# Kernel optimization log

Measured on AMD Instinct MI355X. Metric: run time of the kernel, lower is better.

Reference implementation:

```python
import jax, jax.numpy as jnp
import numpy as np

TAU = 0.1

def setup_inputs() -> dict:
    key = jax.random.key(0)
    kZ, k1, k2 = jax.random.split(key, 3)
    N, D = 8192, 128
    scale = 1.0 / np.sqrt(D)
    return {
        "Z": jax.random.normal(kZ, (N, D), dtype=jnp.float32),
        "W1": jax.random.normal(k1, (D, D), dtype=jnp.float32) * scale,
        "b1": jnp.zeros((D,), dtype=jnp.float32),
        "W2": jax.random.normal(k2, (D, D), dtype=jnp.float32) * scale,
        "b2": jnp.zeros((D,), dtype=jnp.float32),
    }

def reference(Z, W1, b1, W2, b2):
    # DiffusivityTransform: 2-layer MLP with ReLU (torch Linear: x @ W.T + b;
    # here W1/W2 are stored already transposed as [in, out])
    t = jax.nn.relu(Z @ W1 + b1) @ W2 + b2          # [N, D]
    sim = t @ t.T                                     # [N, N]
    S = jax.nn.softmax(sim, axis=1)                   # row-stochastic [N, N]
    Z_prop = S @ Z                                    # [N, D]
    return Z + TAU * (Z_prop - Z)
```

## Files before the change

kernel.cpp:

```cpp
#include <hip/hip_runtime.h>

typedef _Float16 half_t;
typedef _Float16 hx8 __attribute__((ext_vector_type(8)));
typedef _Float16 hx4 __attribute__((ext_vector_type(4)));
typedef float fx4 __attribute__((ext_vector_type(4)));

#define LOG2E 1.44269504088896f
#define TAU 0.1f
#define NSPLIT 8

__global__ __launch_bounds__(256) void mlpz_kernel(
    const float* __restrict__ Z, const float* __restrict__ W1,
    const float* __restrict__ b1, const float* __restrict__ W2,
    const float* __restrict__ b2, half_t* __restrict__ T,
    half_t* __restrict__ Zth)
{
  __shared__ float Ztile[64*132];
  __shared__ half_t Hs[4][16*136];
  const int tid = threadIdx.x;
  const int w = tid >> 6, lane = tid & 63;
  const int q = lane >> 4, c = lane & 15;
  const int rb = blockIdx.x*64;
  const int wrow = rb + w*16;

#pragma unroll
  for (int i=0;i<8;++i) {
    int fid = i*256 + tid;
    int r = fid >> 5, c4 = (fid & 31)*4;
    *(fx4*)(&Ztile[r*132 + c4]) = *(const fx4*)(Z + (size_t)(rb + r)*128 + c4);
  }
  __syncthreads();

  {
    const int d = tid >> 1, n0 = (tid & 1)*32;
#pragma unroll
    for (int i=0;i<4;++i) {
      hx8 hv;
#pragma unroll
      for (int u=0;u<8;++u) hv[u] = (half_t)Ztile[(n0 + i*8 + u)*132 + d];
      *(hx8*)(Zth + (size_t)d*8192 + rb + n0 + i*8) = hv;
    }
  }

  hx8 zb[4];
#pragma unroll
  for (int ks=0;ks<4;++ks) {
    fx4 a = *(const fx4*)(&Ztile[(w*16 + c)*132 + ks*32 + q*8]);
    fx4 b = *(const fx4*)(&Ztile[(w*16 + c)*132 + ks*32 + q*8 + 4]);
#pragma unroll
    for (int u=0;u<4;++u) { zb[ks][u] = (half_t)a[u]; zb[ks][4+u] = (half_t)b[u]; }
  }

  fx4 acc[8];
#pragma unroll
  for (int mt=0;mt<8;++mt) acc[mt] = (fx4){0.f,0.f,0.f,0.f};
#pragma unroll
  for (int mt=0;mt<8;++mt)
#pragma unroll
    for (int ks=0;ks<4;++ks) {
      hx8 aw;
#pragma unroll
      for (int j=0;j<8;++j)
        aw[j] = (half_t)W1[(size_t)(ks*32 + q*8 + j)*128 + mt*16 + c];
      acc[mt] = __builtin_amdgcn_mfma_f32_16x16x32_f16(aw, zb[ks], acc[mt], 0,0,0);
    }
#pragma unroll
  for (int mt=0;mt<8;++mt) {
    fx4 bias = *(const fx4*)(b1 + mt*16 + 4*q);
    hx4 hv;
#pragma unroll
    for (int i=0;i<4;++i) {
      float h = acc[mt][i] + bias[i];
      hv[i] = (half_t)(h > 0.f ? h : 0.f);
    }
    *(hx4*)(&Hs[w][c*136 + mt*16 + 4*q]) = hv;
  }

  hx8 hb[4];
#pragma unroll
  for (int ks=0;ks<4;++ks) hb[ks] = *(const hx8*)(&Hs[w][c*136 + ks*32 + q*8]);
#pragma unroll
  for (int mt=0;mt<8;++mt) acc[mt] = (fx4){0.f,0.f,0.f,0.f};
#pragma unroll
  for (int mt=0;mt<8;++mt)
#pragma unroll
    for (int ks=0;ks<4;++ks) {
      hx8 aw;
#pragma unroll
      for (int j=0;j<8;++j)
        aw[j] = (half_t)W2[(size_t)(ks*32 + q*8 + j)*128 + mt*16 + c];
      acc[mt] = __builtin_amdgcn_mfma_f32_16x16x32_f16(aw, hb[ks], acc[mt], 0,0,0);
    }
#pragma unroll
  for (int mt=0;mt<8;++mt) {
    fx4 bias = *(const fx4*)(b2 + mt*16 + 4*q);
    hx4 tv;
#pragma unroll
    for (int i=0;i<4;++i) tv[i] = (half_t)(acc[mt][i] + bias[i]);
    *(hx4*)(T + (size_t)(wrow + c)*128 + mt*16 + 4*q) = tv;
  }
}

__global__ __launch_bounds__(256,2) void flash_kernel(
    const half_t* __restrict__ T, const half_t* __restrict__ Zt,
    half_t* __restrict__ Pacc, float* __restrict__ Pm, float* __restrict__ Pl)
{
  __shared__ half_t Tbuf[2][16*512];
  __shared__ half_t Zbuf[2][16*512];
  const int tid = threadIdx.x;
  const int w = tid >> 6, lane = tid & 63;
  const int q = lane >> 4, c = lane & 15;
  const int bx = blockIdx.x;
  const int qb = bx >> 3, kh = bx & 7;
  const int wrow = qb*128 + w*32;
  const int sw = (c & 7) * 8;

  hx8 bq[2][4];
#pragma unroll
  for (int nt=0;nt<2;++nt)
#pragma unroll
    for (int ks=0;ks<4;++ks)
      bq[nt][ks] = *(const hx8*)(T + (size_t)(wrow + nt*16 + c)*128 + ks*32 + q*8);

  fx4 oacc[8][2];
#pragma unroll
  for (int mtd=0;mtd<8;++mtd)
#pragma unroll
    for (int nt=0;nt<2;++nt) oacc[mtd][nt] = (fx4){0.f,0.f,0.f,0.f};
  float m_run[2] = {-1e30f,-1e30f};
  float l_run[2] = {0.f,0.f};

  const int kbase = kh*1024;

  auto issue_loads = [&](int kt0, int b) {
    if (w < 2) {
#pragma unroll
      for (int i=0;i<8;++i) {
        int f = w*8 + i, mt = f >> 2, ks = f & 3;
        const half_t* gp = T + (size_t)(kt0 + mt*16 + c)*128 + ks*32 + q*8;
        half_t* lp = &Tbuf[b][f*512 + lane*8];
        __builtin_amdgcn_global_load_lds(
            (const __attribute__((address_space(1))) void*)gp,
            (__attribute__((address_space(3))) void*)lp, 16, 0, 0);
      }
    } else {
#pragma unroll
      for (int i=0;i<8;++i) {
        int f2 = (w-2)*8 + i, mtd = f2 >> 1, ks2 = f2 & 1;
        const half_t* gp = Zt + (size_t)(mtd*16 + c)*8192 + kt0 + ks2*32 + q*8;
        half_t* lp = &Zbuf[b][f2*512 + lane*8];
        __builtin_amdgcn_global_load_lds(
            (const __attribute__((address_space(1))) void*)gp,
            (__attribute__((address_space(3))) void*)lp, 16, 0, 0);
      }
    }
  };

  issue_loads(kbase, 0);

  for (int t=0;t<16;++t) {
    const int cur = t & 1;
    __syncthreads();
    half_t* Tcur = Tbuf[cur];
    half_t* Zcur = Zbuf[cur];
    half_t* Psw  = &Tbuf[cur][w*2048];

    fx4 sacc[4][2];
#pragma unroll
    for (int mt=0;mt<4;++mt)
#pragma unroll
      for (int nt=0;nt<2;++nt) sacc[mt][nt] = (fx4){0.f,0.f,0.f,0.f};
#pragma unroll
    for (int ks=0;ks<4;++ks)
#pragma unroll
      for (int mt=0;mt<4;++mt) {
        hx8 ak = *(const hx8*)(&Tcur[(mt*4+ks)*512 + lane*8]);
        sacc[mt][0] = __builtin_amdgcn_mfma_f32_16x16x32_f16(ak, bq[0][ks], sacc[mt][0], 0,0,0);
        sacc[mt][1] = __builtin_amdgcn_mfma_f32_16x16x32_f16(ak, bq[1][ks], sacc[mt][1], 0,0,0);
      }

    hx4 pk[2][4];
#pragma unroll
    for (int nt=0;nt<2;++nt) {
      float mx = -1e30f;
#pragma unroll
      for (int mt=0;mt<4;++mt)
#pragma unroll
        for (int i=0;i<4;++i) mx = fmaxf(mx, sacc[mt][nt][i]);
      mx = fmaxf(mx, __shfl_xor(mx, 16, 64));
      mx = fmaxf(mx, __shfl_xor(mx, 32, 64));
      float mnew = fmaxf(m_run[nt], mx);
      float alpha = __builtin_amdgcn_exp2f((m_run[nt]-mnew)*LOG2E);
      m_run[nt] = mnew;
      float nb = mnew*LOG2E;
      float rs = 0.f;
#pragma unroll
      for (int mt=0;mt<4;++mt) {
#pragma unroll
        for (int i=0;i<4;++i) {
          float p = __builtin_amdgcn_exp2f(sacc[mt][nt][i]*LOG2E - nb);
          rs += p;
          pk[nt][mt][i] = (half_t)p;
        }
      }
      rs += __shfl_xor(rs, 16, 64);
      rs += __shfl_xor(rs, 32, 64);
      l_run[nt] = l_run[nt]*alpha + rs;
#pragma unroll
      for (int mtd=0;mtd<8;++mtd)
#pragma unroll
        for (int i=0;i<4;++i) oacc[mtd][nt][i] *= alpha;
    }

    __syncthreads();
    if (t < 15) issue_loads(kbase + (t+1)*64, cur ^ 1);

#pragma unroll
    for (int nt=0;nt<2;++nt)
#pragma unroll
      for (int mt=0;mt<4;++mt)
        *(hx4*)(&Psw[(nt*16 + c)*64 + ((mt*16 + 4*q) ^ sw)]) = pk[nt][mt];

#pragma unroll
    for (int ks2=0;ks2<2;++ks2) {
      hx8 bp0 = *(const hx8*)(&Psw[(c     )*64 + ((ks2*32 + q*8) ^ sw)]);
      hx8 bp1 = *(const hx8*)(&Psw[(16 + c)*64 + ((ks2*32 + q*8) ^ sw)]);
#pragma unroll
      for (int mtd=0;mtd<8;++mtd) {
        hx8 az = *(const hx8*)(&Zcur[(mtd*2+ks2)*512 + lane*8]);
        oacc[mtd][0] = __builtin_amdgcn_mfma_f32_16x16x32_f16(az, bp0, oacc[mtd][0], 0,0,0);
        oacc[mtd][1] = __builtin_amdgcn_mfma_f32_16x16x32_f16(az, bp1, oacc[mtd][1], 0,0,0);
      }
    }
  }

#pragma unroll
  for (int nt=0;nt<2;++nt) {
    float inv = 1.0f / l_run[nt];
    const size_t rowg = (size_t)(bx*128 + w*32 + nt*16 + c);
#pragma unroll
    for (int mtd=0;mtd<8;++mtd) {
      hx4 ov;
#pragma unroll
      for (int i=0;i<4;++i) ov[i] = (half_t)(oacc[mtd][nt][i]*inv);
      *(hx4*)(Pacc + rowg*128 + mtd*16 + 4*q) = ov;
    }
    if (q == 0) {
      Pm[rowg] = m_run[nt];
      Pl[rowg] = l_run[nt];
    }
  }
}

__global__ __launch_bounds__(256) void merge_kernel(
    const float* __restrict__ Z, const half_t* __restrict__ Pacc,
    const float* __restrict__ Pm, const float* __restrict__ Pl,
    float* __restrict__ out)
{
  const int th = blockIdx.x*256 + threadIdx.x;
  const int r = th >> 5, cg = th & 31;
  const int qb = r >> 7, rr = r & 127;
  float mk[NSPLIT], lk[NSPLIT];
  float M = -1e30f;
#pragma unroll
  for (int k=0;k<NSPLIT;++k) {
    int p = qb*NSPLIT + k;
    mk[k] = Pm[p*128 + rr];
    lk[k] = Pl[p*128 + rr];
    M = fmaxf(M, mk[k]);
  }
  float L = 0.f, wk[NSPLIT];
#pragma unroll
  for (int k=0;k<NSPLIT;++k) { wk[k] = lk[k]*__builtin_amdgcn_exp2f((mk[k]-M)*LOG2E); L += wk[k]; }
  float o0=0.f,o1=0.f,o2=0.f,o3=0.f;
#pragma unroll
  for (int k=0;k<NSPLIT;++k) {
    int p = qb*NSPLIT + k;
    hx4 v = *(const hx4*)(Pacc + ((size_t)p*128 + rr)*128 + cg*4);
    o0 += wk[k]*(float)v[0]; o1 += wk[k]*(float)v[1];
    o2 += wk[k]*(float)v[2]; o3 += wk[k]*(float)v[3];
  }
  float invL = 1.0f / L;
  fx4 zv = *(const fx4*)(Z + (size_t)r*128 + cg*4);
  fx4 res;
  res[0] = (1.f-TAU)*zv[0] + TAU*o0*invL;
  res[1] = (1.f-TAU)*zv[1] + TAU*o1*invL;
  res[2] = (1.f-TAU)*zv[2] + TAU*o2*invL;
  res[3] = (1.f-TAU)*zv[3] + TAU*o3*invL;
  *(fx4*)(out + (size_t)r*128 + cg*4) = res;
}

extern "C" void kernel_launch(void* const* d_in, const int* in_sizes, int n_in,
                              void* d_out, int out_size, void* d_ws, size_t ws_size,
                              hipStream_t stream) {
  const float* Z  = (const float*)d_in[0];
  const float* W1 = (const float*)d_in[1];
  const float* b1 = (const float*)d_in[2];
  const float* W2 = (const float*)d_in[3];
  const float* b2 = (const float*)d_in[4];
  float* out = (float*)d_out;

  char* ws = (char*)d_ws;
  const size_t NBLK = 64 * NSPLIT;
  half_t* Thi  = (half_t*)(ws);
  half_t* Zth  = (half_t*)(ws + (size_t)2*1024*1024);
  half_t* Pacc = (half_t*)(ws + (size_t)4*1024*1024);
  float*  Pm   = (float*)(ws + (size_t)4*1024*1024 + NBLK*128*128*2);
  float*  Pl   = Pm + NBLK*128;

  hipLaunchKernelGGL(mlpz_kernel,  dim3(128),  dim3(256), 0, stream, Z, W1, b1, W2, b2, Thi, Zth);
  hipLaunchKernelGGL(flash_kernel, dim3(NBLK), dim3(256), 0, stream, Thi, Zth, Pacc, Pm, Pl);
  hipLaunchKernelGGL(merge_kernel, dim3(1024), dim3(256), 0, stream, Z, Pacc, Pm, Pl, out);
}
```

Before: 131.0 us.

## Split T/Z prefetch across all waves and drop mid-loop barrier

Tile loads are now split evenly across all four waves instead of two waves each, and issued separately. The next T tile is issued right after the score MFMAs and the next Z tile midway through the PV MFMAs. The P scratch buffer moves from the current T buffer to each wave's own slice of the next Z buffer, which removes the second __syncthreads per iteration. This relies on each wave's P slice lining up with the Z region that same wave loads, and on its P reads finishing before the async LDS load overwrites them.

```diff
diff --git a/kernel.cpp b/kernel.cpp
--- a/kernel.cpp
+++ b/kernel.cpp
@@ -132,38 +132,38 @@
 
   const int kbase = kh*1024;
 
-  auto issue_loads = [&](int kt0, int b) {
-    if (w < 2) {
-#pragma unroll
-      for (int i=0;i<8;++i) {
-        int f = w*8 + i, mt = f >> 2, ks = f & 3;
-        const half_t* gp = T + (size_t)(kt0 + mt*16 + c)*128 + ks*32 + q*8;
-        half_t* lp = &Tbuf[b][f*512 + lane*8];
-        __builtin_amdgcn_global_load_lds(
-            (const __attribute__((address_space(1))) void*)gp,
-            (__attribute__((address_space(3))) void*)lp, 16, 0, 0);
-      }
-    } else {
-#pragma unroll
-      for (int i=0;i<8;++i) {
-        int f2 = (w-2)*8 + i, mtd = f2 >> 1, ks2 = f2 & 1;
-        const half_t* gp = Zt + (size_t)(mtd*16 + c)*8192 + kt0 + ks2*32 + q*8;
-        half_t* lp = &Zbuf[b][f2*512 + lane*8];
-        __builtin_amdgcn_global_load_lds(
-            (const __attribute__((address_space(1))) void*)gp,
-            (__attribute__((address_space(3))) void*)lp, 16, 0, 0);
-      }
+  auto issue_T = [&](int kt0, int b) {
+#pragma unroll
+    for (int i=0;i<4;++i) {
+      int f = w*4 + i, mt = f >> 2, ks = f & 3;
+      const half_t* gp = T + (size_t)(kt0 + mt*16 + c)*128 + ks*32 + q*8;
+      half_t* lp = &Tbuf[b][f*512 + lane*8];
+      __builtin_amdgcn_global_load_lds(
+          (const __attribute__((address_space(1))) void*)gp,
+          (__attribute__((address_space(3))) void*)lp, 16, 0, 0);
     }
   };
-
-  issue_loads(kbase, 0);
+  auto issue_Z = [&](int kt0, int b) {
+#pragma unroll
+    for (int i=0;i<4;++i) {
+      int f2 = w*4 + i, mtd = f2 >> 1, ks2 = f2 & 1;
+      const half_t* gp = Zt + (size_t)(mtd*16 + c)*8192 + kt0 + ks2*32 + q*8;
+      half_t* lp = &Zbuf[b][f2*512 + lane*8];
+      __builtin_amdgcn_global_load_lds(
+          (const __attribute__((address_space(1))) void*)gp,
+          (__attribute__((address_space(3))) void*)lp, 16, 0, 0);
+    }
+  };
+
+  issue_T(kbase, 0);
+  issue_Z(kbase, 0);
 
   for (int t=0;t<16;++t) {
     const int cur = t & 1;
     __syncthreads();
     half_t* Tcur = Tbuf[cur];
     half_t* Zcur = Zbuf[cur];
-    half_t* Psw  = &Tbuf[cur][w*2048];
+    half_t* Psw  = &Zbuf[cur ^ 1][w*2048];
 
     fx4 sacc[4][2];
 #pragma unroll
@@ -178,6 +178,7 @@
         sacc[mt][0] = __builtin_amdgcn_mfma_f32_16x16x32_f16(ak, bq[0][ks], sacc[mt][0], 0,0,0);
         sacc[mt][1] = __builtin_amdgcn_mfma_f32_16x16x32_f16(ak, bq[1][ks], sacc[mt][1], 0,0,0);
       }
+    if (t < 15) issue_T(kbase + (t+1)*64, cur ^ 1);
 
     hx4 pk[2][4];
 #pragma unroll
@@ -212,26 +213,36 @@
         for (int i=0;i<4;++i) oacc[mtd][nt][i] *= alpha;
     }
 
-    __syncthreads();
-    if (t < 15) issue_loads(kbase + (t+1)*64, cur ^ 1);
-
 #pragma unroll
     for (int nt=0;nt<2;++nt)
 #pragma unroll
       for (int mt=0;mt<4;++mt)
         *(hx4*)(&Psw[(nt*16 + c)*64 + ((mt*16 + 4*q) ^ sw)]) = pk[nt][mt];
 
+    hx8 bp[2][2];
 #pragma unroll
     for (int ks2=0;ks2<2;++ks2) {
-      hx8 bp0 = *(const hx8*)(&Psw[(c     )*64 + ((ks2*32 + q*8) ^ sw)]);
-      hx8 bp1 = *(const hx8*)(&Psw[(16 + c)*64 + ((ks2*32 + q*8) ^ sw)]);
-#pragma unroll
-      for (int mtd=0;mtd<8;++mtd) {
+      bp[ks2][0] = *(const hx8*)(&Psw[(c     )*64 + ((ks2*32 + q*8) ^ sw)]);
+      bp[ks2][1] = *(const hx8*)(&Psw[(16 + c)*64 + ((ks2*32 + q*8) ^ sw)]);
+    }
+
+#pragma unroll
+    for (int ks2=0;ks2<2;++ks2)
+#pragma unroll
+      for (int mtd=0;mtd<4;++mtd) {
         hx8 az = *(const hx8*)(&Zcur[(mtd*2+ks2)*512 + lane*8]);
-        oacc[mtd][0] = __builtin_amdgcn_mfma_f32_16x16x32_f16(az, bp0, oacc[mtd][0], 0,0,0);
-        oacc[mtd][1] = __builtin_amdgcn_mfma_f32_16x16x32_f16(az, bp1, oacc[mtd][1], 0,0,0);
+        oacc[mtd][0] = __builtin_amdgcn_mfma_f32_16x16x32_f16(az, bp[ks2][0], oacc[mtd][0], 0,0,0);
+        oacc[mtd][1] = __builtin_amdgcn_mfma_f32_16x16x32_f16(az, bp[ks2][1], oacc[mtd][1], 0,0,0);
       }
-    }
+    if (t < 15) issue_Z(kbase + (t+1)*64, cur ^ 1);
+#pragma unroll
+    for (int ks2=0;ks2<2;++ks2)
+#pragma unroll
+      for (int mtd=4;mtd<8;++mtd) {
+        hx8 az = *(const hx8*)(&Zcur[(mtd*2+ks2)*512 + lane*8]);
+        oacc[mtd][0] = __builtin_amdgcn_mfma_f32_16x16x32_f16(az, bp[ks2][0], oacc[mtd][0], 0,0,0);
+        oacc[mtd][1] = __builtin_amdgcn_mfma_f32_16x16x32_f16(az, bp[ks2][1], oacc[mtd][1], 0,0,0);
+      }
   }
 
 #pragma unroll
```

Result: no change. 132.4 us (+1.1%).
